# Kernel tuning notes

Hardware: AMD Instinct MI355X
Metric: run time of the kernel (lower is better)

## Reference

```python
import jax, jax.numpy as jnp
import numpy as np

QMAX = 127.0  # 2**(bits-1) - 1 for bits=8, signed symmetric


def _quantize_signed_symmetric(t):
    # per-tensor symmetric: scale = max|t| / qmax, q = clamp(round(t/scale))
    scale = jnp.max(jnp.abs(t)) / QMAX
    q = jnp.clip(jnp.round(t / scale), -QMAX, QMAX)
    return q, scale


def setup_inputs() -> dict:
    key = jax.random.key(0)
    k1, k2, k3 = jax.random.split(key, 3)
    N, D_IN, D_OUT = 16384, 1024, 1024
    x = jax.random.normal(k1, (N, D_IN), dtype=jnp.float32)
    weight = jax.random.normal(k2, (D_OUT, D_IN), dtype=jnp.float32) * 0.02
    bias = jax.random.normal(k3, (D_OUT,), dtype=jnp.float32) * 0.01
    return {"x": x, "weight": weight, "bias": bias}


def reference(x, weight, bias):
    # weight quantization (cached in torch; recomputed here, same math)
    qw, w_scale = _quantize_signed_symmetric(weight)
    qw_t = qw.astype(jnp.int32).T            # [D_IN, D_OUT]
    # activation quantization
    qx, x_scale = _quantize_signed_symmetric(x)
    qx = qx.astype(jnp.int32)                # [N, D_IN]
    # int32 matmul, then per-tensor dequant + bias
    acc = qx @ qw_t                          # int32 [N, D_OUT]
    y = acc.astype(jnp.float32) * (x_scale * w_scale)
    return y + bias
```

## Files before the change

kernel.cpp:

```cpp
#include <hip/hip_runtime.h>

#define QMAX 127.0f
#define BM 128
#define BN 128
#define BK 64

typedef int int4v __attribute__((ext_vector_type(4)));
typedef float float4v __attribute__((ext_vector_type(4)));

__global__ void absmax2_kernel(const float4* __restrict__ px, int n4x,
                               const float4* __restrict__ pw, int n4w,
                               int gx, int* __restrict__ amax) {
    const float4* p; int n4; int* out; int nb, bid;
    if ((int)blockIdx.x < gx) { p = px; n4 = n4x; out = amax + 0; nb = gx; bid = blockIdx.x; }
    else { p = pw; n4 = n4w; out = amax + 1; nb = gridDim.x - gx; bid = blockIdx.x - gx; }
    float m = 0.f;
    int stride = nb * blockDim.x;
    for (int i = bid * blockDim.x + threadIdx.x; i < n4; i += stride) {
        float4 v = p[i];
        m = fmaxf(m, fmaxf(fmaxf(fabsf(v.x), fabsf(v.y)),
                           fmaxf(fabsf(v.z), fabsf(v.w))));
    }
    for (int off = 32; off; off >>= 1) m = fmaxf(m, __shfl_down(m, off, 64));
    __shared__ float sm[4];
    if ((threadIdx.x & 63) == 0) sm[threadIdx.x >> 6] = m;
    __syncthreads();
    if (threadIdx.x == 0) {
        float b = fmaxf(fmaxf(sm[0], sm[1]), fmaxf(sm[2], sm[3]));
        atomicMax(out, (int)__float_as_uint(b));
    }
}

__device__ __forceinline__ int qone(float v, float s) {
    float q = fminf(fmaxf(rintf(v / s), -QMAX), QMAX);
    return (int)q;
}
__device__ __forceinline__ int qpack4(float4 v, float s) {
    return (qone(v.x, s) & 255) | ((qone(v.y, s) & 255) << 8) |
           ((qone(v.z, s) & 255) << 16) | ((qone(v.w, s) & 255) << 24);
}

__global__ void quant2_kernel(const float4* __restrict__ sx, int4v* __restrict__ dx, int n16x,
                              const float4* __restrict__ sw, int4v* __restrict__ dw, int n16w,
                              int gx, const int* __restrict__ amax) {
    const float4* src; int4v* dst; int n16, nb, bid; float scale;
    if ((int)blockIdx.x < gx) {
        src = sx; dst = dx; n16 = n16x; nb = gx; bid = blockIdx.x;
        scale = __uint_as_float((unsigned)amax[0]) / QMAX;
    } else {
        src = sw; dst = dw; n16 = n16w; nb = gridDim.x - gx; bid = blockIdx.x - gx;
        scale = __uint_as_float((unsigned)amax[1]) / QMAX;
    }
    int stride = nb * blockDim.x;
    for (int i = bid * blockDim.x + threadIdx.x; i < n16; i += stride) {
        float4 v0 = src[4 * i + 0];
        float4 v1 = src[4 * i + 1];
        float4 v2 = src[4 * i + 2];
        float4 v3 = src[4 * i + 3];
        int4v o = { qpack4(v0, scale), qpack4(v1, scale),
                    qpack4(v2, scale), qpack4(v3, scale) };
        dst[i] = o;
    }
}

typedef const __attribute__((address_space(1))) char glob_char;
typedef __attribute__((address_space(3))) char lds_char;

__device__ __forceinline__ void gload16(const char* g, char* l) {
    __builtin_amdgcn_global_load_lds((glob_char*)g, (lds_char*)l, 16, 0, 0);
}

__global__ __launch_bounds__(256, 4) void gemm_i8_kernel(
        const char* __restrict__ qa, const char* __restrict__ qb,
        const float4* __restrict__ bias4, const int* __restrict__ amax,
        float* __restrict__ out, int M, int N, int K, int nbx) {
    __shared__ char sA[2][BM * BK];
    __shared__ char sB[2][BN * BK];

    const int b = blockIdx.x;
    const int chunk = gridDim.x >> 3;
    const int s = (b & 7) * chunk + (b >> 3);
    const int mt = s / nbx, nt = s % nbx;

    const int tid = threadIdx.x;
    const int lane = tid & 63;
    const int wid = tid >> 6;
    const int wm = wid >> 1, wn = wid & 1;
    const int m0 = mt * BM, n0 = nt * BN;

    const int L0 = tid, L1 = 256 + tid;
    const int row0 = ((L0 >> 6) << 4) + (L0 & 15);
    const int col0 = ((L0 >> 4) & 3) << 4;
    const int row1 = ((L1 >> 6) << 4) + (L1 & 15);
    const int col1 = ((L1 >> 4) & 3) << 4;

    const char* gA0 = qa + (size_t)(m0 + row0) * K + col0;
    const char* gA1 = qa + (size_t)(m0 + row1) * K + col1;
    const char* gB0 = qb + (size_t)(n0 + row0) * K + col0;
    const char* gB1 = qb + (size_t)(n0 + row1) * K + col1;

    int4v acc[4][4];
    const int4v zero = {0, 0, 0, 0};
#pragma unroll
    for (int i = 0; i < 4; ++i)
#pragma unroll
        for (int j = 0; j < 4; ++j) acc[i][j] = zero;

    const int aoff = wm * 4 * 64 + lane;
    const int boff = wn * 4 * 64 + lane;
    const int NI = K / BK;

    gload16(gA0, sA[0] + L0 * 16);
    gload16(gA1, sA[0] + L1 * 16);
    gload16(gB0, sB[0] + L0 * 16);
    gload16(gB1, sB[0] + L1 * 16);
    gA0 += BK; gA1 += BK; gB0 += BK; gB1 += BK;

    for (int k0 = 0; k0 < NI; ++k0) {
        const int cur = k0 & 1;
        __syncthreads();

        if (k0 + 1 < NI) {
            const int nxt = cur ^ 1;
            gload16(gA0, sA[nxt] + L0 * 16);
            gload16(gA1, sA[nxt] + L1 * 16);
            gload16(gB0, sB[nxt] + L0 * 16);
            gload16(gB1, sB[nxt] + L1 * 16);
            gA0 += BK; gA1 += BK; gB0 += BK; gB1 += BK;
        }

        const int4v* sAv = (const int4v*)sA[cur];
        const int4v* sBv = (const int4v*)sB[cur];
        int4v a[4], bfr[4];
#pragma unroll
        for (int t = 0; t < 4; ++t) {
            a[t] = sAv[aoff + t * 64];
            bfr[t] = sBv[boff + t * 64];
        }
#pragma unroll
        for (int j = 0; j < 4; ++j)
#pragma unroll
            for (int i = 0; i < 4; ++i)
                acc[j][i] = __builtin_amdgcn_mfma_i32_16x16x64_i8(bfr[j], a[i], acc[j][i], 0, 0, 0);
    }

    const float sc = (__uint_as_float((unsigned)amax[0]) / QMAX) *
                     (__uint_as_float((unsigned)amax[1]) / QMAX);
    const int quad = lane >> 4;
    const int rbase = m0 + wm * 64 + (lane & 15);
    const int cb_e = n0 + wn * 64;
#pragma unroll
    for (int j = 0; j < 4; ++j) {
        const int colv = (cb_e >> 2) + (j << 2) + quad;
        const float4 bv = bias4[colv];
#pragma unroll
        for (int i = 0; i < 4; ++i) {
            const int row = rbase + i * 16;
            float4v v;
            v[0] = (float)acc[j][i][0] * sc + bv.x;
            v[1] = (float)acc[j][i][1] * sc + bv.y;
            v[2] = (float)acc[j][i][2] * sc + bv.z;
            v[3] = (float)acc[j][i][3] * sc + bv.w;
            float4v* dst = (float4v*)(out + (size_t)row * N) + colv;
            __builtin_nontemporal_store(v, dst);
        }
    }
}

extern "C" void kernel_launch(void* const* d_in, const int* in_sizes, int n_in,
                              void* d_out, int out_size, void* d_ws, size_t ws_size,
                              hipStream_t stream) {
    const float* x = (const float*)d_in[0];
    const float* w = (const float*)d_in[1];
    const float* bias = (const float*)d_in[2];
    float* out = (float*)d_out;

    const int xn = in_sizes[0];
    const int wn = in_sizes[1];
    const int N = in_sizes[2];
    const int K = wn / N;
    const int M = xn / K;

    int* amax = (int*)d_ws;
    char* qx = (char*)d_ws + 1024;
    char* qw = qx + (size_t)M * K;

    const int GAX = 2048, GAW = 256;
    absmax2_kernel<<<GAX + GAW, 256, 0, stream>>>(
        (const float4*)x, xn / 4, (const float4*)w, wn / 4, GAX, amax);

    const int GQX = 4096, GQW = 256;
    quant2_kernel<<<GQX + GQW, 256, 0, stream>>>(
        (const float4*)x, (int4v*)qx, xn / 16,
        (const float4*)w, (int4v*)qw, wn / 16, GQX, amax);

    const int nbx = N / BN;
    gemm_i8_kernel<<<nbx * (M / BM), 256, 0, stream>>>(
        qx, qw, (const float4*)bias, amax, out, M, N, K, nbx);
}
```

Measured before the change: 185.2 us.

## Restructure int8 GEMM: full-K A tile in LDS, prepacked weights streamed from global

The quantize kernel now writes the int8 weight in a pre-swizzled MFMA fragment layout. The GEMM gives each 512-thread block 64 rows of A and all N columns. The block loads the whole 64xK A panel into LDS once, and each wave streams its 128 B columns from global memory straight into registers with double buffering. This removes the per-k-step LDS staging and barriers for B and the repeated A reloads across N tiles. In exchange it uses 64 KB of dynamic LDS, holds 128 accumulator registers per lane, relies on L2 for B reuse across blocks, and drops the nontemporal output stores.

```diff
diff --git a/kernel.cpp b/kernel.cpp
--- a/kernel.cpp
+++ b/kernel.cpp
@@ -1,9 +1,6 @@
 #include <hip/hip_runtime.h>
 
 #define QMAX 127.0f
-#define BM 128
-#define BN 128
-#define BK 64
 
 typedef int int4v __attribute__((ext_vector_type(4)));
 typedef float float4v __attribute__((ext_vector_type(4)));
@@ -42,13 +39,13 @@
 
 __global__ void quant2_kernel(const float4* __restrict__ sx, int4v* __restrict__ dx, int n16x,
                               const float4* __restrict__ sw, int4v* __restrict__ dw, int n16w,
-                              int gx, const int* __restrict__ amax) {
-    const float4* src; int4v* dst; int n16, nb, bid; float scale;
+                              int gx, int kshift, int KC, const int* __restrict__ amax) {
+    const float4* src; int n16, nb, bid; float scale; int isw;
     if ((int)blockIdx.x < gx) {
-        src = sx; dst = dx; n16 = n16x; nb = gx; bid = blockIdx.x;
+        src = sx; n16 = n16x; nb = gx; bid = blockIdx.x; isw = 0;
         scale = __uint_as_float((unsigned)amax[0]) / QMAX;
     } else {
-        src = sw; dst = dw; n16 = n16w; nb = gridDim.x - gx; bid = blockIdx.x - gx;
+        src = sw; n16 = n16w; nb = gridDim.x - gx; bid = blockIdx.x - gx; isw = 1;
         scale = __uint_as_float((unsigned)amax[1]) / QMAX;
     }
     int stride = nb * blockDim.x;
@@ -59,7 +56,15 @@
         float4 v3 = src[4 * i + 3];
         int4v o = { qpack4(v0, scale), qpack4(v1, scale),
                     qpack4(v2, scale), qpack4(v3, scale) };
-        dst[i] = o;
+        if (!isw) {
+            dx[i] = o;
+        } else {
+            int n = i >> kshift;
+            int kg = i & ((1 << kshift) - 1);
+            int kc = kg >> 2, q = kg & 3;
+            int g = n >> 4, r = n & 15;
+            dw[(g * KC + kc) * 64 + q * 16 + r] = o;
+        }
     }
 }
 
@@ -70,89 +75,81 @@
     __builtin_amdgcn_global_load_lds((glob_char*)g, (lds_char*)l, 16, 0, 0);
 }
 
-__global__ __launch_bounds__(256, 4) void gemm_i8_kernel(
+__global__ __launch_bounds__(512, 2) void gemm_i8_kernel(
         const char* __restrict__ qa, const char* __restrict__ qb,
         const float4* __restrict__ bias4, const int* __restrict__ amax,
-        float* __restrict__ out, int M, int N, int K, int nbx) {
-    __shared__ char sA[2][BM * BK];
-    __shared__ char sB[2][BN * BK];
+        float* __restrict__ out, int M, int N, int K) {
+    extern __shared__ char sA[];
 
-    const int b = blockIdx.x;
-    const int chunk = gridDim.x >> 3;
-    const int s = (b & 7) * chunk + (b >> 3);
-    const int mt = s / nbx, nt = s % nbx;
-
+    const int KC = K >> 6;
     const int tid = threadIdx.x;
     const int lane = tid & 63;
-    const int wid = tid >> 6;
-    const int wm = wid >> 1, wn = wid & 1;
-    const int m0 = mt * BM, n0 = nt * BN;
+    const int w = tid >> 6;
+    const int m0 = blockIdx.x * 64;
+    const int kb = __builtin_ctz(K);
 
-    const int L0 = tid, L1 = 256 + tid;
-    const int row0 = ((L0 >> 6) << 4) + (L0 & 15);
-    const int col0 = ((L0 >> 4) & 3) << 4;
-    const int row1 = ((L1 >> 6) << 4) + (L1 & 15);
-    const int col1 = ((L1 >> 4) & 3) << 4;
+    const int rounds = (K >> 3) >> 2;
+    for (int R = 0; R < rounds; ++R) {
+        const int C = R * 512 + tid;
+        const int i = C >> kb;
+        const int kc = (C & (K - 1)) >> 6;
+        const int q = (C >> 4) & 3;
+        const int r = C & 15;
+        const char* src = qa + (size_t)(m0 + i * 16 + r) * K + kc * 64 + q * 16;
+        gload16(src, sA + (size_t)C * 16);
+    }
+    __syncthreads();
 
-    const char* gA0 = qa + (size_t)(m0 + row0) * K + col0;
-    const char* gA1 = qa + (size_t)(m0 + row1) * K + col1;
-    const char* gB0 = qb + (size_t)(n0 + row0) * K + col0;
-    const char* gB1 = qb + (size_t)(n0 + row1) * K + col1;
-
-    int4v acc[4][4];
+    int4v acc[8][4];
     const int4v zero = {0, 0, 0, 0};
 #pragma unroll
-    for (int i = 0; i < 4; ++i)
+    for (int j = 0; j < 8; ++j)
 #pragma unroll
-        for (int j = 0; j < 4; ++j) acc[i][j] = zero;
+        for (int i = 0; i < 4; ++i) acc[j][i] = zero;
 
-    const int aoff = wm * 4 * 64 + lane;
-    const int boff = wn * 4 * 64 + lane;
-    const int NI = K / BK;
+    const int4v* sAv = (const int4v*)sA;
+    const char* bbase = qb + (size_t)(w * 8) * KC * 1024 + lane * 16;
 
-    gload16(gA0, sA[0] + L0 * 16);
-    gload16(gA1, sA[0] + L1 * 16);
-    gload16(gB0, sB[0] + L0 * 16);
-    gload16(gB1, sB[0] + L1 * 16);
-    gA0 += BK; gA1 += BK; gB0 += BK; gB1 += BK;
+#define LOADB(Bb, kc)                                                        \
+    do { _Pragma("unroll") for (int j = 0; j < 8; ++j)                       \
+        Bb[j] = *(const int4v*)(bbase + ((size_t)j * KC + (kc)) * 1024);     \
+    } while (0)
+#define LOADA(Af, kc)                                                        \
+    do { _Pragma("unroll") for (int i = 0; i < 4; ++i)                       \
+        Af[i] = sAv[i * K + (kc) * 64 + lane];                               \
+    } while (0)
+#define MF(Bb, Af)                                                           \
+    do { _Pragma("unroll") for (int j = 0; j < 8; ++j)                       \
+        _Pragma("unroll") for (int i = 0; i < 4; ++i)                        \
+            acc[j][i] = __builtin_amdgcn_mfma_i32_16x16x64_i8(               \
+                Bb[j], Af[i], acc[j][i], 0, 0, 0);                           \
+    } while (0)
 
-    for (int k0 = 0; k0 < NI; ++k0) {
-        const int cur = k0 & 1;
-        __syncthreads();
-
-        if (k0 + 1 < NI) {
-            const int nxt = cur ^ 1;
-            gload16(gA0, sA[nxt] + L0 * 16);
-            gload16(gA1, sA[nxt] + L1 * 16);
-            gload16(gB0, sB[nxt] + L0 * 16);
-            gload16(gB1, sB[nxt] + L1 * 16);
-            gA0 += BK; gA1 += BK; gB0 += BK; gB1 += BK;
-        }
-
-        const int4v* sAv = (const int4v*)sA[cur];
-        const int4v* sBv = (const int4v*)sB[cur];
-        int4v a[4], bfr[4];
-#pragma unroll
-        for (int t = 0; t < 4; ++t) {
-            a[t] = sAv[aoff + t * 64];
-            bfr[t] = sBv[boff + t * 64];
-        }
-#pragma unroll
-        for (int j = 0; j < 4; ++j)
-#pragma unroll
-            for (int i = 0; i < 4; ++i)
-                acc[j][i] = __builtin_amdgcn_mfma_i32_16x16x64_i8(bfr[j], a[i], acc[j][i], 0, 0, 0);
+    int4v B0[8], B1[8], Af[4];
+    LOADB(B0, 0);
+#pragma unroll 1
+    for (int kc = 0; kc + 2 < KC; kc += 2) {
+        LOADB(B1, kc + 1);
+        LOADA(Af, kc);
+        MF(B0, Af);
+        LOADB(B0, kc + 2);
+        LOADA(Af, kc + 1);
+        MF(B1, Af);
     }
+    LOADB(B1, KC - 1);
+    LOADA(Af, KC - 2);
+    MF(B0, Af);
+    LOADA(Af, KC - 1);
+    MF(B1, Af);
 
     const float sc = (__uint_as_float((unsigned)amax[0]) / QMAX) *
                      (__uint_as_float((unsigned)amax[1]) / QMAX);
     const int quad = lane >> 4;
-    const int rbase = m0 + wm * 64 + (lane & 15);
-    const int cb_e = n0 + wn * 64;
+    const int rbase = m0 + (lane & 15);
+    const int cb4 = w * 32;
 #pragma unroll
-    for (int j = 0; j < 4; ++j) {
-        const int colv = (cb_e >> 2) + (j << 2) + quad;
-        const float4 bv = bias4[colv];
+    for (int j = 0; j < 8; ++j) {
+        const float4 bv = bias4[cb4 + j * 4 + quad];
 #pragma unroll
         for (int i = 0; i < 4; ++i) {
             const int row = rbase + i * 16;
@@ -161,8 +158,7 @@
             v[1] = (float)acc[j][i][1] * sc + bv.y;
             v[2] = (float)acc[j][i][2] * sc + bv.z;
             v[3] = (float)acc[j][i][3] * sc + bv.w;
-            float4v* dst = (float4v*)(out + (size_t)row * N) + colv;
-            __builtin_nontemporal_store(v, dst);
+            *((float4v*)(out + (size_t)row * N) + cb4 + j * 4 + quad) = v;
         }
     }
 }
@@ -180,6 +176,8 @@
     const int N = in_sizes[2];
     const int K = wn / N;
     const int M = xn / K;
+    const int KC = K >> 6;
+    const int kshift = __builtin_ctz(K >> 4);
 
     int* amax = (int*)d_ws;
     char* qx = (char*)d_ws + 1024;
@@ -192,9 +190,8 @@
     const int GQX = 4096, GQW = 256;
     quant2_kernel<<<GQX + GQW, 256, 0, stream>>>(
         (const float4*)x, (int4v*)qx, xn / 16,
-        (const float4*)w, (int4v*)qw, wn / 16, GQX, amax);
+        (const float4*)w, (int4v*)qw, wn / 16, GQX, kshift, KC, amax);
 
-    const int nbx = N / BN;
-    gemm_i8_kernel<<<nbx * (M / BM), 256, 0, stream>>>(
-        qx, qw, (const float4*)bias, amax, out, M, N, K, nbx);
+    gemm_i8_kernel<<<M / 64, 512, 64 * K, stream>>>(
+        qx, qw, (const float4*)bias, amax, out, M, N, K);
 }
```

New measurement: 175.2 us. 5.4% less time.
